# Kernel optimization log

Measured on AMD Instinct MI355X. Metric: run time of the kernel, lower is better.

Reference implementation:

```python
import jax, jax.numpy as jnp
import numpy as np
from jax import lax


def setup_inputs() -> dict:
    key = jax.random.key(0)
    ks = jax.random.split(key, 5)
    B, Cin, H, W = 16, 64, 64, 64
    HID, K = 128, 3
    x = jax.random.normal(ks[0], (B, Cin, H, W), jnp.float32)
    w_is = jax.random.normal(ks[1], (4 * HID, Cin, 1, K), jnp.float32) * 0.05
    b_is = jax.random.normal(ks[2], (4 * HID,), jnp.float32) * 0.05
    w_ss = jax.random.normal(ks[3], (4 * HID, HID, 1, K), jnp.float32) * 0.05
    b_ss = jax.random.normal(ks[4], (4 * HID,), jnp.float32) * 0.05
    return {"x": x, "w_is": w_is, "b_is": b_is, "w_ss": w_ss, "b_ss": b_ss}


def reference(x, w_is, b_is, w_ss, b_ss):
    # Shapes: x [B,Cin,H,W]; w_is [4h,Cin,1,k]; w_ss [4h,h,1,k]
    hid = w_ss.shape[1]
    k = w_is.shape[-1]
    pad = k // 2

    # MaskedConv2d mask type 'B' on a (1,k) kernel: keep center and left taps,
    # zero everything strictly right of center.
    mask = (jnp.arange(k) <= pad).astype(x.dtype)  # [k]
    w_is_m = w_is * mask[None, None, None, :]

    # Input-to-state conv over the whole image at once: [B,4h,H,W]
    z_is = lax.conv_general_dilated(
        x, w_is_m, window_strides=(1, 1), padding=[(0, 0), (pad, pad)]
    ) + b_is[None, :, None, None]

    # State-to-state conv is a 1D conv along W: kernel [4h, h, k]
    w1 = w_ss[:, :, 0, :]

    def step(carry, z_row):
        h, c = carry  # each [B, hid, W]
        z = z_row + lax.conv_general_dilated(
            h, w1, window_strides=(1,), padding=[(pad, pad)],
            dimension_numbers=("NCH", "OIH", "NCH"),
        ) + b_ss[None, :, None]
        i_g = jax.nn.sigmoid(z[:, :hid])
        f_g = jax.nn.sigmoid(z[:, hid:2 * hid])
        o_g = jax.nn.sigmoid(z[:, 2 * hid:3 * hid])
        g = jnp.tanh(z[:, 3 * hid:])
        c = f_g * c + i_g * g
        h = o_g * jnp.tanh(c)
        return (h, c), h

    B, _, H, W = x.shape
    h0 = jnp.zeros((B, hid, W), x.dtype)
    c0 = jnp.zeros((B, hid, W), x.dtype)
    zs = jnp.transpose(z_is, (2, 0, 1, 3))  # [H, B, 4h, W]
    _, hs = lax.scan(step, (h0, c0), zs)    # hs: [H, B, hid, W]
    return jnp.transpose(hs, (1, 2, 0, 3))  # [B, hid, H, W]
```

## Files before the change

kernel.cpp:

```cpp
#include <hip/hip_runtime.h>
#include <hip/hip_bf16.h>

#define B_    16
#define CIN   64
#define Hn    64
#define Wn    64
#define HID   128
#define SXS2  72
#define SHS   136

typedef __attribute__((ext_vector_type(8))) short bfrag_t;
typedef __attribute__((ext_vector_type(4))) float f4_t;

#define HBUF_SHORTS (B_ * Wn * HID)
#define HBUF_BYTES  (HBUF_SHORTS * 2)
#define CNT_STRIDE  256

static __device__ __forceinline__ short f2bf(float f) {
    union { __hip_bfloat16 h; short s; } u;
    u.h = __float2bfloat16(f);
    return u.s;
}

extern "C" __global__ __launch_bounds__(256, 1)
void rowlstm_kernel(const float* __restrict__ x,
                    const float* __restrict__ w_is,
                    const float* __restrict__ b_is,
                    const float* __restrict__ w_ss,
                    const float* __restrict__ b_ss,
                    float* __restrict__ out,
                    unsigned char* __restrict__ ws)
{
    const int tid  = threadIdx.x;
    const int bid  = blockIdx.x;
    const int b    = bid & 15;
    const int jc   = bid >> 4;
    const int lane = tid & 63;
    const int wv   = tid >> 6;
    const int l15  = lane & 15;
    const int quad = lane >> 4;

    short*    hbuf0 = (short*)ws;
    unsigned* cnt   = (unsigned*)(ws + 2 * HBUF_BYTES + b * CNT_STRIDE);

    __shared__ alignas(16) short sH[66 * SHS];
    __shared__ alignas(16) short sX2[65 * SXS2];
    __shared__ float sZ[32 * 66];
    __shared__ float sBias[32];

    if (tid < 32) {
        int g = tid >> 3, r = tid & 7;
        int co = g * HID + jc * 8 + r;
        sBias[tid] = b_is[co] + b_ss[co];
    }

    bfrag_t a_frag[2][16];
    #pragma unroll
    for (int mt = 0; mt < 2; ++mt) {
        int lr = mt * 16 + l15;
        int g = lr >> 3, r = lr & 7;
        int co = g * HID + jc * 8 + r;
        #pragma unroll
        for (int kt = 0; kt < 16; ++kt) {
            bfrag_t v;
            #pragma unroll
            for (int j = 0; j < 8; ++j) {
                int kk = kt * 32 + quad * 8 + j;
                float val;
                if      (kk < 64)  val = w_is[(co * CIN + kk) * 3 + 0];
                else if (kk < 128) val = w_is[(co * CIN + (kk - 64)) * 3 + 1];
                else if (kk < 256) val = w_ss[(co * HID + (kk - 128)) * 3 + 0];
                else if (kk < 384) val = w_ss[(co * HID + (kk - 256)) * 3 + 1];
                else               val = w_ss[(co * HID + (kk - 384)) * 3 + 2];
                v[j] = f2bf(val);
            }
            a_frag[mt][kt] = v;
        }
    }

    {
        bfrag_t z8 = {0,0,0,0,0,0,0,0};
        if (tid < 8)  *(bfrag_t*)&sX2[tid * 8] = z8;
        if (tid < 16) {
            *(bfrag_t*)&sH[tid * 8] = z8;
            *(bfrag_t*)&sH[65 * SHS + tid * 8] = z8;
        }
    }

    float creg[2] = {0.f, 0.f};
    const int w_c = tid & 63;
    const int jl2 = tid >> 6;

    const int xw  = tid & 63;
    const int xc2 = tid >> 6;
    float xr[16];
    #pragma unroll
    for (int e = 0; e < 16; ++e)
        xr[e] = x[((b * CIN + xc2 * 16 + e) * Hn + 0) * Wn + xw];

    __syncthreads();

    for (int h = 0; h < Hn; ++h) {
        const short* rd_hb = hbuf0 + ((h & 1) ^ 1) * HBUF_SHORTS + b * Wn * HID;
        short*       wr_hb = hbuf0 + (h & 1) * HBUF_SHORTS + b * Wn * HID;

        {
            bfrag_t v0, v1;
            #pragma unroll
            for (int e = 0; e < 8; ++e) { v0[e] = f2bf(xr[e]); v1[e] = f2bf(xr[e + 8]); }
            *(bfrag_t*)&sX2[(xw + 1) * SXS2 + xc2 * 16]     = v0;
            *(bfrag_t*)&sX2[(xw + 1) * SXS2 + xc2 * 16 + 8] = v1;
        }
        {
            int cig = tid & 15, w0 = tid >> 4;
            #pragma unroll
            for (int it = 0; it < 4; ++it) {
                int w = w0 + it * 16;
                union { bfrag_t f; unsigned long long q[2]; } u;
                if (h == 0) { u.q[0] = 0ull; u.q[1] = 0ull; }
                else {
                    const unsigned long long* src =
                        (const unsigned long long*)(rd_hb + w * HID + cig * 8);
                    u.q[0] = __hip_atomic_load(src,     __ATOMIC_RELAXED, __HIP_MEMORY_SCOPE_AGENT);
                    u.q[1] = __hip_atomic_load(src + 1, __ATOMIC_RELAXED, __HIP_MEMORY_SCOPE_AGENT);
                }
                *(bfrag_t*)&sH[(w + 1) * SHS + cig * 8] = u.f;
            }
        }
        __syncthreads();

        f4_t acc0 = {0.f, 0.f, 0.f, 0.f};
        f4_t acc1 = {0.f, 0.f, 0.f, 0.f};
        const int wp = wv * 16 + l15;
        #pragma unroll
        for (int kt = 0; kt < 16; ++kt) {
            const short* src;
            if (kt < 4) {
                src = &sX2[(wp + (kt >> 1)) * SXS2 + (kt & 1) * 32 + quad * 8];
            } else {
                src = &sH[(wp + ((kt - 4) >> 2)) * SHS + ((kt - 4) & 3) * 32 + quad * 8];
            }
            bfrag_t bf = *(const bfrag_t*)src;
            acc0 = __builtin_amdgcn_mfma_f32_16x16x32_bf16(a_frag[0][kt], bf, acc0, 0, 0, 0);
            acc1 = __builtin_amdgcn_mfma_f32_16x16x32_bf16(a_frag[1][kt], bf, acc1, 0, 0, 0);
        }
        #pragma unroll
        for (int r = 0; r < 4; ++r) {
            sZ[(quad * 4 + r) * 66      + wp] = acc0[r];
            sZ[(16 + quad * 4 + r) * 66 + wp] = acc1[r];
        }
        __syncthreads();

        {
            float hv2[2];
            #pragma unroll
            for (int it = 0; it < 2; ++it) {
                int jl = jl2 * 2 + it;
                float z0 = sZ[(jl) * 66 + w_c]      + sBias[jl];
                float z1 = sZ[(8 + jl) * 66 + w_c]  + sBias[8 + jl];
                float z2 = sZ[(16 + jl) * 66 + w_c] + sBias[16 + jl];
                float z3 = sZ[(24 + jl) * 66 + w_c] + sBias[24 + jl];
                float ig = 1.f / (1.f + __expf(-z0));
                float fg = 1.f / (1.f + __expf(-z1));
                float og = 1.f / (1.f + __expf(-z2));
                float gg = 2.f / (1.f + __expf(-2.f * z3)) - 1.f;
                float c  = fg * creg[it] + ig * gg;
                creg[it] = c;
                float th = 2.f / (1.f + __expf(-2.f * c)) - 1.f;
                hv2[it]  = og * th;
                out[((b * HID + jc * 8 + jl) * Hn + h) * Wn + w_c] = hv2[it];
            }
            unsigned pk = (unsigned)(unsigned short)f2bf(hv2[0]) |
                          ((unsigned)(unsigned short)f2bf(hv2[1]) << 16);
            unsigned* dst = (unsigned*)(wr_hb + w_c * HID + jc * 8 + jl2 * 2);
            __hip_atomic_store(dst, pk, __ATOMIC_RELAXED, __HIP_MEMORY_SCOPE_AGENT);
        }
        {
            int hp = (h < Hn - 1) ? h + 1 : h;
            #pragma unroll
            for (int e = 0; e < 16; ++e)
                xr[e] = x[((b * CIN + xc2 * 16 + e) * Hn + hp) * Wn + xw];
        }
        __syncthreads();

        if (h < Hn - 1) {
            if (tid == 0) {
                __hip_atomic_fetch_add(cnt, 1u, __ATOMIC_RELAXED, __HIP_MEMORY_SCOPE_AGENT);
                unsigned target = (unsigned)(16 * (h + 1));
                while (__hip_atomic_load(cnt, __ATOMIC_RELAXED, __HIP_MEMORY_SCOPE_AGENT) < target)
                    __builtin_amdgcn_s_sleep(2);
            }
            __syncthreads();
        }
    }
}

extern "C" void kernel_launch(void* const* d_in, const int* in_sizes, int n_in,
                              void* d_out, int out_size, void* d_ws, size_t ws_size,
                              hipStream_t stream) {
    const float* x    = (const float*)d_in[0];
    const float* w_is = (const float*)d_in[1];
    const float* b_is = (const float*)d_in[2];
    const float* w_ss = (const float*)d_in[3];
    const float* b_ss = (const float*)d_in[4];
    float* out = (float*)d_out;
    unsigned char* ws = (unsigned char*)d_ws;

    hipMemsetAsync(ws + 2 * HBUF_BYTES, 0, B_ * CNT_STRIDE, stream);

    rowlstm_kernel<<<dim3(256), dim3(256), 0, stream>>>(x, w_is, b_is, w_ss, b_ss, out, ws);
}
```

Baseline: 320.0 us.

## Halve blocks, keep gate math in registers, split barrier into arrive/wait

Each block now covers 16 hidden channels instead of 8, so 128 blocks with 4 MFMA accumulators replace 256 blocks with 2. Gate nonlinearities are applied straight to the accumulator registers, which removes the sZ shared buffer and one block-wide sync per row. The inter-block counter barrier becomes arrive-after-store and wait-before-load, with all threads polling. The next x row is prefetched earlier. Risks are higher register pressure from 64 A fragments, and the removed __syncthreads before the first loop plus relaxed memory ordering on the counter could cause races.

```diff
diff --git a/kernel.cpp b/kernel.cpp
--- a/kernel.cpp
+++ b/kernel.cpp
@@ -8,6 +8,8 @@
 #define HID   128
 #define SXS2  72
 #define SHS   136
+#define NJC   8
+#define NBLK  (B_ * NJC)
 
 typedef __attribute__((ext_vector_type(8))) short bfrag_t;
 typedef __attribute__((ext_vector_type(4))) float f4_t;
@@ -21,6 +23,8 @@
     u.h = __float2bfloat16(f);
     return u.s;
 }
+static __device__ __forceinline__ float sigm(float z)  { return 1.f / (1.f + __expf(-z)); }
+static __device__ __forceinline__ float tanhf_(float z){ return 2.f / (1.f + __expf(-2.f * z)) - 1.f; }
 
 extern "C" __global__ __launch_bounds__(256, 1)
 void rowlstm_kernel(const float* __restrict__ x,
@@ -45,36 +49,34 @@
 
     __shared__ alignas(16) short sH[66 * SHS];
     __shared__ alignas(16) short sX2[65 * SXS2];
-    __shared__ float sZ[32 * 66];
-    __shared__ float sBias[32];
-
-    if (tid < 32) {
-        int g = tid >> 3, r = tid & 7;
-        int co = g * HID + jc * 8 + r;
-        sBias[tid] = b_is[co] + b_ss[co];
-    }
-
-    bfrag_t a_frag[2][16];
+
+    bfrag_t a_frag[4][16];
     #pragma unroll
-    for (int mt = 0; mt < 2; ++mt) {
-        int lr = mt * 16 + l15;
-        int g = lr >> 3, r = lr & 7;
-        int co = g * HID + jc * 8 + r;
+    for (int mt = 0; mt < 4; ++mt) {
+        const int co = mt * HID + jc * 16 + l15;
         #pragma unroll
         for (int kt = 0; kt < 16; ++kt) {
+            const int kk0 = kt * 32 + quad * 8;
+            const float* p;
+            if      (kt < 2)  p = &w_is[(co * CIN + kk0)         * 3 + 0];
+            else if (kt < 4)  p = &w_is[(co * CIN + (kk0 - 64))  * 3 + 1];
+            else if (kt < 8)  p = &w_ss[(co * HID + (kk0 - 128)) * 3 + 0];
+            else if (kt < 12) p = &w_ss[(co * HID + (kk0 - 256)) * 3 + 1];
+            else              p = &w_ss[(co * HID + (kk0 - 384)) * 3 + 2];
             bfrag_t v;
             #pragma unroll
-            for (int j = 0; j < 8; ++j) {
-                int kk = kt * 32 + quad * 8 + j;
-                float val;
-                if      (kk < 64)  val = w_is[(co * CIN + kk) * 3 + 0];
-                else if (kk < 128) val = w_is[(co * CIN + (kk - 64)) * 3 + 1];
-                else if (kk < 256) val = w_ss[(co * HID + (kk - 128)) * 3 + 0];
-                else if (kk < 384) val = w_ss[(co * HID + (kk - 256)) * 3 + 1];
-                else               val = w_ss[(co * HID + (kk - 384)) * 3 + 2];
-                v[j] = f2bf(val);
-            }
+            for (int j = 0; j < 8; ++j) v[j] = f2bf(p[j * 3]);
             a_frag[mt][kt] = v;
+        }
+    }
+
+    float bias[4][4];
+    #pragma unroll
+    for (int g = 0; g < 4; ++g) {
+        #pragma unroll
+        for (int r = 0; r < 4; ++r) {
+            const int co = g * HID + jc * 16 + quad * 4 + r;
+            bias[g][r] = b_is[co] + b_ss[co];
         }
     }
 
@@ -87,9 +89,8 @@
         }
     }
 
-    float creg[2] = {0.f, 0.f};
-    const int w_c = tid & 63;
-    const int jl2 = tid >> 6;
+    float creg[4] = {0.f, 0.f, 0.f, 0.f};
+    const int wp  = wv * 16 + l15;
 
     const int xw  = tid & 63;
     const int xc2 = tid >> 6;
@@ -98,11 +99,38 @@
     for (int e = 0; e < 16; ++e)
         xr[e] = x[((b * CIN + xc2 * 16 + e) * Hn + 0) * Wn + xw];
 
-    __syncthreads();
+    const int cig = tid & 15;
+    const int w0  = tid >> 4;
 
     for (int h = 0; h < Hn; ++h) {
         const short* rd_hb = hbuf0 + ((h & 1) ^ 1) * HBUF_SHORTS + b * Wn * HID;
         short*       wr_hb = hbuf0 + (h & 1) * HBUF_SHORTS + b * Wn * HID;
+
+        if (h > 0) {
+            const unsigned target = (unsigned)(NJC * h);
+            while (__hip_atomic_load(cnt, __ATOMIC_RELAXED, __HIP_MEMORY_SCOPE_AGENT) < target)
+                __builtin_amdgcn_s_sleep(1);
+            asm volatile("" ::: "memory");
+        }
+
+        union { bfrag_t f; unsigned long long q[2]; } hu0, hu1, hu2, hu3;
+        if (h > 0) {
+            const unsigned long long* s0 = (const unsigned long long*)(rd_hb + (w0 +  0) * HID + cig * 8);
+            const unsigned long long* s1 = (const unsigned long long*)(rd_hb + (w0 + 16) * HID + cig * 8);
+            const unsigned long long* s2 = (const unsigned long long*)(rd_hb + (w0 + 32) * HID + cig * 8);
+            const unsigned long long* s3 = (const unsigned long long*)(rd_hb + (w0 + 48) * HID + cig * 8);
+            hu0.q[0] = __hip_atomic_load(s0,     __ATOMIC_RELAXED, __HIP_MEMORY_SCOPE_AGENT);
+            hu0.q[1] = __hip_atomic_load(s0 + 1, __ATOMIC_RELAXED, __HIP_MEMORY_SCOPE_AGENT);
+            hu1.q[0] = __hip_atomic_load(s1,     __ATOMIC_RELAXED, __HIP_MEMORY_SCOPE_AGENT);
+            hu1.q[1] = __hip_atomic_load(s1 + 1, __ATOMIC_RELAXED, __HIP_MEMORY_SCOPE_AGENT);
+            hu2.q[0] = __hip_atomic_load(s2,     __ATOMIC_RELAXED, __HIP_MEMORY_SCOPE_AGENT);
+            hu2.q[1] = __hip_atomic_load(s2 + 1, __ATOMIC_RELAXED, __HIP_MEMORY_SCOPE_AGENT);
+            hu3.q[0] = __hip_atomic_load(s3,     __ATOMIC_RELAXED, __HIP_MEMORY_SCOPE_AGENT);
+            hu3.q[1] = __hip_atomic_load(s3 + 1, __ATOMIC_RELAXED, __HIP_MEMORY_SCOPE_AGENT);
+        } else {
+            hu0.q[0] = hu0.q[1] = 0ull; hu1.q[0] = hu1.q[1] = 0ull;
+            hu2.q[0] = hu2.q[1] = 0ull; hu3.q[0] = hu3.q[1] = 0ull;
+        }
 
         {
             bfrag_t v0, v1;
@@ -112,26 +140,20 @@
             *(bfrag_t*)&sX2[(xw + 1) * SXS2 + xc2 * 16 + 8] = v1;
         }
         {
-            int cig = tid & 15, w0 = tid >> 4;
+            const int hp = (h < Hn - 1) ? h + 1 : h;
             #pragma unroll
-            for (int it = 0; it < 4; ++it) {
-                int w = w0 + it * 16;
-                union { bfrag_t f; unsigned long long q[2]; } u;
-                if (h == 0) { u.q[0] = 0ull; u.q[1] = 0ull; }
-                else {
-                    const unsigned long long* src =
-                        (const unsigned long long*)(rd_hb + w * HID + cig * 8);
-                    u.q[0] = __hip_atomic_load(src,     __ATOMIC_RELAXED, __HIP_MEMORY_SCOPE_AGENT);
-                    u.q[1] = __hip_atomic_load(src + 1, __ATOMIC_RELAXED, __HIP_MEMORY_SCOPE_AGENT);
-                }
-                *(bfrag_t*)&sH[(w + 1) * SHS + cig * 8] = u.f;
-            }
-        }
+            for (int e = 0; e < 16; ++e)
+                xr[e] = x[((b * CIN + xc2 * 16 + e) * Hn + hp) * Wn + xw];
+        }
+        *(bfrag_t*)&sH[(w0 +  1) * SHS + cig * 8] = hu0.f;
+        *(bfrag_t*)&sH[(w0 + 17) * SHS + cig * 8] = hu1.f;
+        *(bfrag_t*)&sH[(w0 + 33) * SHS + cig * 8] = hu2.f;
+        *(bfrag_t*)&sH[(w0 + 49) * SHS + cig * 8] = hu3.f;
+
         __syncthreads();
 
-        f4_t acc0 = {0.f, 0.f, 0.f, 0.f};
-        f4_t acc1 = {0.f, 0.f, 0.f, 0.f};
-        const int wp = wv * 16 + l15;
+        f4_t acc0 = {0.f,0.f,0.f,0.f}, acc1 = {0.f,0.f,0.f,0.f};
+        f4_t acc2 = {0.f,0.f,0.f,0.f}, acc3 = {0.f,0.f,0.f,0.f};
         #pragma unroll
         for (int kt = 0; kt < 16; ++kt) {
             const short* src;
@@ -143,55 +165,36 @@
             bfrag_t bf = *(const bfrag_t*)src;
             acc0 = __builtin_amdgcn_mfma_f32_16x16x32_bf16(a_frag[0][kt], bf, acc0, 0, 0, 0);
             acc1 = __builtin_amdgcn_mfma_f32_16x16x32_bf16(a_frag[1][kt], bf, acc1, 0, 0, 0);
-        }
+            acc2 = __builtin_amdgcn_mfma_f32_16x16x32_bf16(a_frag[2][kt], bf, acc2, 0, 0, 0);
+            acc3 = __builtin_amdgcn_mfma_f32_16x16x32_bf16(a_frag[3][kt], bf, acc3, 0, 0, 0);
+        }
+
+        float hv[4];
         #pragma unroll
         for (int r = 0; r < 4; ++r) {
-            sZ[(quad * 4 + r) * 66      + wp] = acc0[r];
-            sZ[(16 + quad * 4 + r) * 66 + wp] = acc1[r];
-        }
+            float ig = sigm (acc0[r] + bias[0][r]);
+            float fg = sigm (acc1[r] + bias[1][r]);
+            float og = sigm (acc2[r] + bias[2][r]);
+            float gg = tanhf_(acc3[r] + bias[3][r]);
+            float c  = fg * creg[r] + ig * gg;
+            creg[r]  = c;
+            hv[r]    = og * tanhf_(c);
+            out[((b * HID + jc * 16 + quad * 4 + r) * Hn + h) * Wn + wp] = hv[r];
+        }
+        {
+            unsigned p0 = (unsigned)(unsigned short)f2bf(hv[0]) |
+                          ((unsigned)(unsigned short)f2bf(hv[1]) << 16);
+            unsigned p1 = (unsigned)(unsigned short)f2bf(hv[2]) |
+                          ((unsigned)(unsigned short)f2bf(hv[3]) << 16);
+            unsigned long long pk = (unsigned long long)p0 | ((unsigned long long)p1 << 32);
+            unsigned long long* dst = (unsigned long long*)(wr_hb + wp * HID + jc * 16 + quad * 4);
+            __hip_atomic_store(dst, pk, __ATOMIC_RELAXED, __HIP_MEMORY_SCOPE_AGENT);
+        }
+
         __syncthreads();
 
-        {
-            float hv2[2];
-            #pragma unroll
-            for (int it = 0; it < 2; ++it) {
-                int jl = jl2 * 2 + it;
-                float z0 = sZ[(jl) * 66 + w_c]      + sBias[jl];
-                float z1 = sZ[(8 + jl) * 66 + w_c]  + sBias[8 + jl];
-                float z2 = sZ[(16 + jl) * 66 + w_c] + sBias[16 + jl];
-                float z3 = sZ[(24 + jl) * 66 + w_c] + sBias[24 + jl];
-                float ig = 1.f / (1.f + __expf(-z0));
-                float fg = 1.f / (1.f + __expf(-z1));
-                float og = 1.f / (1.f + __expf(-z2));
-                float gg = 2.f / (1.f + __expf(-2.f * z3)) - 1.f;
-                float c  = fg * creg[it] + ig * gg;
-                creg[it] = c;
-                float th = 2.f / (1.f + __expf(-2.f * c)) - 1.f;
-                hv2[it]  = og * th;
-                out[((b * HID + jc * 8 + jl) * Hn + h) * Wn + w_c] = hv2[it];
-            }
-            unsigned pk = (unsigned)(unsigned short)f2bf(hv2[0]) |
-                          ((unsigned)(unsigned short)f2bf(hv2[1]) << 16);
-            unsigned* dst = (unsigned*)(wr_hb + w_c * HID + jc * 8 + jl2 * 2);
-            __hip_atomic_store(dst, pk, __ATOMIC_RELAXED, __HIP_MEMORY_SCOPE_AGENT);
-        }
-        {
-            int hp = (h < Hn - 1) ? h + 1 : h;
-            #pragma unroll
-            for (int e = 0; e < 16; ++e)
-                xr[e] = x[((b * CIN + xc2 * 16 + e) * Hn + hp) * Wn + xw];
-        }
-        __syncthreads();
-
-        if (h < Hn - 1) {
-            if (tid == 0) {
-                __hip_atomic_fetch_add(cnt, 1u, __ATOMIC_RELAXED, __HIP_MEMORY_SCOPE_AGENT);
-                unsigned target = (unsigned)(16 * (h + 1));
-                while (__hip_atomic_load(cnt, __ATOMIC_RELAXED, __HIP_MEMORY_SCOPE_AGENT) < target)
-                    __builtin_amdgcn_s_sleep(2);
-            }
-            __syncthreads();
-        }
+        if (h < Hn - 1 && tid == 0)
+            __hip_atomic_fetch_add(cnt, 1u, __ATOMIC_RELAXED, __HIP_MEMORY_SCOPE_AGENT);
     }
 }
 
@@ -208,5 +211,5 @@
 
     hipMemsetAsync(ws + 2 * HBUF_BYTES, 0, B_ * CNT_STRIDE, stream);
 
-    rowlstm_kernel<<<dim3(256), dim3(256), 0, stream>>>(x, w_is, b_is, w_ss, b_ss, out, ws);
+    rowlstm_kernel<<<dim3(NBLK), dim3(256), 0, stream>>>(x, w_is, b_is, w_ss, b_ss, out, ws);
 }
```

Measured after the change: 310.7 us. 1.03x faster.
